# Kernel optimization log

Measured on AMD Instinct MI355X. Metric: run time of the kernel, lower is better.

Reference implementation:

```python
import jax, jax.numpy as jnp
import numpy as np

N_NODES = 100000
IN_FEATS, N_HIDDEN, N_CLASSES = 128, 128, 64
N_EDGES = 1600000


def _glorot(key, shape):
    fan_in, fan_out = shape
    lim = np.sqrt(6.0 / (fan_in + fan_out)).astype(np.float32)
    return jax.random.uniform(key, shape, jnp.float32, -lim, lim)


def setup_inputs() -> dict:
    key = jax.random.key(0)
    ks = jax.random.split(key, 12)
    x = jax.random.normal(ks[0], (N_NODES, IN_FEATS), dtype=jnp.float32)
    src = jax.random.randint(ks[1], (N_EDGES,), 0, N_NODES, dtype=jnp.int32)
    dst = jax.random.randint(ks[2], (N_EDGES,), 0, N_NODES, dtype=jnp.int32)
    dims = [(IN_FEATS, N_HIDDEN), (N_HIDDEN, N_HIDDEN), (N_HIDDEN, N_CLASSES)]
    inp = {"x": x, "src": src, "dst": dst}
    for l, (di, do) in enumerate(dims):
        inp[f"W_self{l}"] = _glorot(ks[3 + 3 * l], (di, do))
        inp[f"W_neigh{l}"] = _glorot(ks[4 + 3 * l], (di, do))
        inp[f"b{l}"] = jnp.zeros((do,), jnp.float32)
    return inp


def _sage_conv(h, src, dst, W_self, W_neigh, b):
    # mean aggregation over incoming neighbors: scatter-sum then divide by degree
    msg = h[src]                                                # [E, d]
    agg = jax.ops.segment_sum(msg, dst, num_segments=N_NODES)   # [N, d]
    deg = jax.ops.segment_sum(jnp.ones((src.shape[0],), h.dtype), dst,
                              num_segments=N_NODES)             # [N]
    h_neigh = agg / jnp.maximum(deg, 1.0)[:, None]
    return h @ W_self + h_neigh @ W_neigh + b


def reference(x, src, dst, W_self0, W_neigh0, b0, W_self1, W_neigh1, b1,
              W_self2, W_neigh2, b2):
    params = [(W_self0, W_neigh0, b0), (W_self1, W_neigh1, b1),
              (W_self2, W_neigh2, b2)]
    h = x
    n_layers = len(params)
    for i, (Ws, Wn, b) in enumerate(params):
        h = _sage_conv(h, src, dst, Ws, Wn, b)
        if i != n_layers - 1:
            h = jax.nn.relu(h)  # dropout is identity in eval mode
    return h
```

## Files before the change

kernel.cpp:

```cpp
#include <hip/hip_runtime.h>
#include <hip/hip_bf16.h>

#define N_NODES 100000
#define N_EDGES 1600000
#define PAD 64
#define FILL_SLICES 8
#define SLICE_NN (N_NODES / FILL_SLICES)
#define FILL_CHUNKS 256
#define CHUNK_E (N_EDGES / FILL_CHUNKS)

#define CVTX_BLOCKS 12500
#define CVTW_BLOCKS 320
#define CINIT_BLOCKS 391

typedef unsigned short ushort_t;
typedef unsigned int uint_t;
typedef __bf16 bf16x8 __attribute__((ext_vector_type(8)));
typedef float f32x4 __attribute__((ext_vector_type(4)));

__device__ __forceinline__ float bf2f_lo(uint_t u) {
    union { uint_t i; float f; } v; v.i = u << 16; return v.f;
}
__device__ __forceinline__ float bf2f_hi(uint_t u) {
    union { uint_t i; float f; } v; v.i = u & 0xffff0000u; return v.f;
}
__device__ __forceinline__ ushort_t f2bf(float f) {
    uint_t x = __float_as_uint(f);
    uint_t r = (x + 0x7fffu + ((x >> 16) & 1u)) >> 16;
    return (ushort_t)r;
}

#define UNPACK4(v) \
    acc[0] += bf2f_lo(v.x); acc[1] += bf2f_hi(v.x); \
    acc[2] += bf2f_lo(v.y); acc[3] += bf2f_hi(v.y); \
    acc[4] += bf2f_lo(v.z); acc[5] += bf2f_hi(v.z); \
    acc[6] += bf2f_lo(v.w); acc[7] += bf2f_hi(v.w);


__global__ __launch_bounds__(256) void k_pre(const float* __restrict__ x, ushort_t* __restrict__ h,
                                             const float* __restrict__ ws0, const float* __restrict__ wn0,
                                             const float* __restrict__ ws1, const float* __restrict__ wn1,
                                             const float* __restrict__ ws2, const float* __restrict__ wn2,
                                             ushort_t* __restrict__ wt0, ushort_t* __restrict__ wt1,
                                             ushort_t* __restrict__ wt2, int* __restrict__ cursor) {
    int b = blockIdx.x;
    if (b < CVTX_BLOCKS) {
        int i = (b * 256 + threadIdx.x) * 4;
        float4 v = *(const float4*)(x + i);
        uint2 o;
        o.x = (uint_t)f2bf(v.x) | ((uint_t)f2bf(v.y) << 16);
        o.y = (uint_t)f2bf(v.z) | ((uint_t)f2bf(v.w) << 16);
        *(uint2*)(h + i) = o;
    } else if (b < CVTX_BLOCKS + CVTW_BLOCKS) {
        int idx = (b - CVTX_BLOCKS) * 256 + threadIdx.x;
        if (idx < 65536) {
            const float* Ws = (idx < 32768) ? ws0 : ws1;
            const float* Wn = (idx < 32768) ? wn0 : wn1;
            ushort_t* Wt    = (idx < 32768) ? wt0 : wt1;
            int local = idx & 32767;
            int n = local >> 8, k = local & 255;
            float v = (k < 128) ? Ws[k * 128 + n] : Wn[(k - 128) * 128 + n];
            Wt[n * 256 + k] = f2bf(v);
        } else {
            int local = idx - 65536;
            int n = local >> 7, k = local & 127;
            float v = (n < 64) ? ws2[k * 64 + n] : wn2[k * 64 + (n - 64)];
            wt2[n * 128 + k] = f2bf(v);
        }
    } else {
        int idx = (b - CVTX_BLOCKS - CVTW_BLOCKS) * 256 + threadIdx.x;
        if (idx < N_NODES) cursor[idx] = idx * PAD;
    }
}


__global__ __launch_bounds__(256) void k_fill(const int* __restrict__ src, const int* __restrict__ dst,
                                              int* __restrict__ cursor, int* __restrict__ colp) {
    int slice = blockIdx.x & (FILL_SLICES - 1);
    int chunk = blockIdx.x >> 3;
    int lo = slice * SLICE_NN, hi = lo + SLICE_NN;
    int base = chunk * CHUNK_E;
    for (int e = base + threadIdx.x; e < base + CHUNK_E; e += 256) {
        int d = dst[e];
        if (d >= lo && d < hi) {
            int s = src[e];
            int p = atomicAdd(&cursor[d], 1);
            colp[p] = s;
        }
    }
}


__global__ __launch_bounds__(256) void k_agg(const ushort_t* __restrict__ h,
                                             const int* __restrict__ cur,
                                             const int* __restrict__ colp,
                                             ushort_t* __restrict__ out) {
    const int node = blockIdx.x * 4 + (threadIdx.x >> 6);
    const int lane = threadIdx.x & 63;
    const int j = lane >> 4;
    const int d = lane & 15;
    const int beg = node * PAD;
    const int end = cur[node];
    float acc[8];
#pragma unroll
    for (int k = 0; k < 8; ++k) acc[k] = 0.f;

    int i = beg;
    for (; i + 16 <= end; i += 16) {
        int c0 = colp[i + j];
        int c1 = colp[i + 4 + j];
        int c2 = colp[i + 8 + j];
        int c3 = colp[i + 12 + j];
        uint4 v0 = *(const uint4*)(h + (size_t)c0 * 128 + d * 8);
        uint4 v1 = *(const uint4*)(h + (size_t)c1 * 128 + d * 8);
        uint4 v2 = *(const uint4*)(h + (size_t)c2 * 128 + d * 8);
        uint4 v3 = *(const uint4*)(h + (size_t)c3 * 128 + d * 8);
        UNPACK4(v0) UNPACK4(v1) UNPACK4(v2) UNPACK4(v3)
    }
    if (i + 8 <= end) {
        int c0 = colp[i + j];
        int c1 = colp[i + 4 + j];
        uint4 v0 = *(const uint4*)(h + (size_t)c0 * 128 + d * 8);
        uint4 v1 = *(const uint4*)(h + (size_t)c1 * 128 + d * 8);
        UNPACK4(v0) UNPACK4(v1)
        i += 8;
    }
    if (i + 4 <= end) {
        int c0 = colp[i + j];
        uint4 v0 = *(const uint4*)(h + (size_t)c0 * 128 + d * 8);
        UNPACK4(v0)
        i += 4;
    }
    int rem = end - i;
    if (rem > 0) {
        int idx = i + (j < rem ? j : 0);
        int c0 = colp[idx];
        uint4 v0 = *(const uint4*)(h + (size_t)c0 * 128 + d * 8);
        if (j < rem) { UNPACK4(v0) }
    }
#pragma unroll
    for (int k = 0; k < 8; ++k) {
        acc[k] += __shfl_xor(acc[k], 16);
        acc[k] += __shfl_xor(acc[k], 32);
    }
    int deg = end - beg;
    float inv = (deg > 0) ? 1.0f / (float)deg : 0.f;
    if (lane < 16) {
        uint4 o;
        o.x = (uint_t)f2bf(acc[0] * inv) | ((uint_t)f2bf(acc[1] * inv) << 16);
        o.y = (uint_t)f2bf(acc[2] * inv) | ((uint_t)f2bf(acc[3] * inv) << 16);
        o.z = (uint_t)f2bf(acc[4] * inv) | ((uint_t)f2bf(acc[5] * inv) << 16);
        o.w = (uint_t)f2bf(acc[6] * inv) | ((uint_t)f2bf(acc[7] * inv) << 16);
        *(uint4*)(out + (size_t)node * 128 + d * 8) = o;
    }
}


__global__ __launch_bounds__(256) void k_agg_add64(const ushort_t* __restrict__ g,
                                                   const int* __restrict__ cur,
                                                   const int* __restrict__ colp,
                                                   float* __restrict__ out) {
    const int node = blockIdx.x * 4 + (threadIdx.x >> 6);
    const int lane = threadIdx.x & 63;
    const int j = lane >> 3;
    const int d = lane & 7;
    const int beg = node * PAD;
    const int end = cur[node];
    float acc[8];
#pragma unroll
    for (int k = 0; k < 8; ++k) acc[k] = 0.f;

    int i = beg;
    for (; i + 16 <= end; i += 16) {
        int c0 = colp[i + j];
        int c1 = colp[i + 8 + j];
        uint4 v0 = *(const uint4*)(g + (size_t)c0 * 64 + d * 8);
        uint4 v1 = *(const uint4*)(g + (size_t)c1 * 64 + d * 8);
        UNPACK4(v0) UNPACK4(v1)
    }
    if (i + 8 <= end) {
        int c0 = colp[i + j];
        uint4 v0 = *(const uint4*)(g + (size_t)c0 * 64 + d * 8);
        UNPACK4(v0)
        i += 8;
    }
    int rem = end - i;
    if (rem > 0) {
        int idx = i + (j < rem ? j : 0);
        int c0 = colp[idx];
        uint4 v0 = *(const uint4*)(g + (size_t)c0 * 64 + d * 8);
        if (j < rem) { UNPACK4(v0) }
    }
#pragma unroll
    for (int k = 0; k < 8; ++k) {
        acc[k] += __shfl_xor(acc[k], 8);
        acc[k] += __shfl_xor(acc[k], 16);
        acc[k] += __shfl_xor(acc[k], 32);
    }
    int deg = end - beg;
    float inv = (deg > 0) ? 1.0f / (float)deg : 0.f;
    if (lane < 8) {
        float* p = out + (size_t)node * 64 + d * 8;
        float4 p0 = *(float4*)p;
        float4 p1 = *(float4*)(p + 4);
        p0.x += acc[0] * inv; p0.y += acc[1] * inv;
        p0.z += acc[2] * inv; p0.w += acc[3] * inv;
        p1.x += acc[4] * inv; p1.y += acc[5] * inv;
        p1.z += acc[6] * inv; p1.w += acc[7] * inv;
        *(float4*)p = p0;
        *(float4*)(p + 4) = p1;
    }
}


__global__ __launch_bounds__(512) void k_gemm(const ushort_t* __restrict__ hs,
                                              const ushort_t* __restrict__ hn,
                                              const ushort_t* __restrict__ wt,
                                              const float* __restrict__ bias,
                                              ushort_t* __restrict__ hout) {
    constexpr int NT = 8;
    __shared__ ushort_t lds_w[128][264];
    const int t = threadIdx.x;
    for (int c = t; c < 128 * 32; c += 512) {
        int r = c >> 5, o = c & 31;
        *(uint4*)(&lds_w[r][o * 8]) = *(const uint4*)(wt + r * 256 + o * 8);
    }
    __syncthreads();

    int wid = t >> 6, lane = t & 63;
    int row0 = blockIdx.x * 128 + wid * 16;
    int arow = row0 + (lane & 15);
    if (arow >= N_NODES) arow = N_NODES - 1;
    int hi = lane >> 4;

    f32x4 acc[NT];
#pragma unroll
    for (int n = 0; n < NT; n++) acc[n] = (f32x4){0.f, 0.f, 0.f, 0.f};

#pragma unroll
    for (int kk = 0; kk < 8; kk++) {
        const ushort_t* hp = (kk < 4) ? hs : hn;
        int kloc = (kk & 3) * 32 + hi * 8;
        bf16x8 a = *(const bf16x8*)(hp + (size_t)arow * 128 + kloc);
#pragma unroll
        for (int n = 0; n < NT; n++) {
            bf16x8 b = *(const bf16x8*)(&lds_w[n * 16 + (lane & 15)][kk * 32 + hi * 8]);
            acc[n] = __builtin_amdgcn_mfma_f32_16x16x32_bf16(a, b, acc[n], 0, 0, 0);
        }
    }

#pragma unroll
    for (int n = 0; n < NT; n++) {
        int colc = n * 16 + (lane & 15);
        float bv = bias[colc];
#pragma unroll
        for (int j = 0; j < 4; j++) {
            int row = row0 + hi * 4 + j;
            if (row < N_NODES) {
                float v = acc[n][j] + bv;
                v = v > 0.f ? v : 0.f;
                hout[(size_t)row * 128 + colc] = f2bf(v);
            }
        }
    }
}


__global__ __launch_bounds__(512) void k_gemm2(const ushort_t* __restrict__ hs,
                                               const ushort_t* __restrict__ wt,
                                               const float* __restrict__ bias,
                                               float* __restrict__ fout,
                                               ushort_t* __restrict__ g2) {
    constexpr int NT = 8;
    __shared__ ushort_t lds_w[128][136];
    const int t = threadIdx.x;
    for (int c = t; c < 128 * 16; c += 512) {
        int r = c >> 4, o = c & 15;
        *(uint4*)(&lds_w[r][o * 8]) = *(const uint4*)(wt + r * 128 + o * 8);
    }
    __syncthreads();

    int wid = t >> 6, lane = t & 63;
    int row0 = blockIdx.x * 128 + wid * 16;
    int arow = row0 + (lane & 15);
    if (arow >= N_NODES) arow = N_NODES - 1;
    int hi = lane >> 4;

    f32x4 acc[NT];
#pragma unroll
    for (int n = 0; n < NT; n++) acc[n] = (f32x4){0.f, 0.f, 0.f, 0.f};

#pragma unroll
    for (int kk = 0; kk < 4; kk++) {
        bf16x8 a = *(const bf16x8*)(hs + (size_t)arow * 128 + kk * 32 + hi * 8);
#pragma unroll
        for (int n = 0; n < NT; n++) {
            bf16x8 b = *(const bf16x8*)(&lds_w[n * 16 + (lane & 15)][kk * 32 + hi * 8]);
            acc[n] = __builtin_amdgcn_mfma_f32_16x16x32_bf16(a, b, acc[n], 0, 0, 0);
        }
    }

#pragma unroll
    for (int n = 0; n < NT; n++) {
        int colc = n * 16 + (lane & 15);
#pragma unroll
        for (int j = 0; j < 4; j++) {
            int row = row0 + hi * 4 + j;
            if (row < N_NODES) {
                float v = acc[n][j];
                if (n < 4) fout[(size_t)row * 64 + colc] = v + bias[colc];
                else       g2[(size_t)row * 64 + (colc - 64)] = f2bf(v);
            }
        }
    }
}


extern "C" void kernel_launch(void* const* d_in, const int* in_sizes, int n_in,
                              void* d_out, int out_size, void* d_ws, size_t ws_size,
                              hipStream_t stream) {
    const float* x   = (const float*)d_in[0];
    const int*   src = (const int*)d_in[1];
    const int*   dst = (const int*)d_in[2];
    const float* ws0 = (const float*)d_in[3];
    const float* wn0 = (const float*)d_in[4];
    const float* b0  = (const float*)d_in[5];
    const float* ws1 = (const float*)d_in[6];
    const float* wn1 = (const float*)d_in[7];
    const float* b1  = (const float*)d_in[8];
    const float* ws2 = (const float*)d_in[9];
    const float* wn2 = (const float*)d_in[10];
    const float* b2  = (const float*)d_in[11];

    char* ws = (char*)d_ws;
    size_t o = 0;
    auto alloc = [&](size_t bytes) { size_t r = o; o = (o + bytes + 255) & ~(size_t)255; return r; };
    int* cursor     = (int*)(ws + alloc((size_t)N_NODES * 4));
    int* colp       = (int*)(ws + alloc((size_t)N_NODES * PAD * 4));
    ushort_t* wt0   = (ushort_t*)(ws + alloc(128 * 256 * 2));
    ushort_t* wt1   = (ushort_t*)(ws + alloc(128 * 256 * 2));
    ushort_t* wt2   = (ushort_t*)(ws + alloc(128 * 128 * 2));
    ushort_t* hA    = (ushort_t*)(ws + alloc((size_t)N_NODES * 128 * 2));
    ushort_t* hB    = (ushort_t*)(ws + alloc((size_t)N_NODES * 128 * 2));
    ushort_t* hN    = (ushort_t*)(ws + alloc((size_t)N_NODES * 128 * 2));
    (void)ws_size;

    k_pre<<<CVTX_BLOCKS + CVTW_BLOCKS + CINIT_BLOCKS, 256, 0, stream>>>(
        x, hA, ws0, wn0, ws1, wn1, ws2, wn2, wt0, wt1, wt2, cursor);
    k_fill<<<FILL_CHUNKS * FILL_SLICES, 256, 0, stream>>>(src, dst, cursor, colp);

    const int AGG_GRID  = N_NODES / 4;
    const int GEMM_GRID = (N_NODES + 127) / 128;

    k_agg<<<AGG_GRID, 256, 0, stream>>>(hA, cursor, colp, hN);
    k_gemm<<<GEMM_GRID, 512, 0, stream>>>(hA, hN, wt0, b0, hB);
    k_agg<<<AGG_GRID, 256, 0, stream>>>(hB, cursor, colp, hN);
    k_gemm<<<GEMM_GRID, 512, 0, stream>>>(hB, hN, wt1, b1, hA);
    k_gemm2<<<GEMM_GRID, 512, 0, stream>>>(hA, wt2, b2, (float*)d_out, hN);
    k_agg_add64<<<AGG_GRID, 256, 0, stream>>>(hN, cursor, colp, (float*)d_out);
}
```

Baseline: 410.4 us.

## Fuse edge fill into preprocessing kernel with memset-initialized degree counters

Replaces the sliced multi-pass fill kernel with a single pass of one thread per edge, merged into the conversion kernel. The cursor array now holds per-node degree counts, zeroed by a memset, instead of absolute offsets. Aggregation kernels compute the end index from the degree. This removes the 8x redundant reads of dst and one kernel launch, but the atomics lose the locality that slicing gave them and fill blocks share the launch with the conversion work. Neighbor order within a node is still nondeterministic.

New measurement: 480.9 us. +17.2%, slower.

```diff
diff --git a/kernel.cpp b/kernel.cpp
--- a/kernel.cpp
+++ b/kernel.cpp
@@ -4,14 +4,10 @@
 #define N_NODES 100000
 #define N_EDGES 1600000
 #define PAD 64
-#define FILL_SLICES 8
-#define SLICE_NN (N_NODES / FILL_SLICES)
-#define FILL_CHUNKS 256
-#define CHUNK_E (N_EDGES / FILL_CHUNKS)
-
+
+#define FILL_BLOCKS 6250
 #define CVTX_BLOCKS 12500
 #define CVTW_BLOCKS 320
-#define CINIT_BLOCKS 391
 
 typedef unsigned short ushort_t;
 typedef unsigned int uint_t;
@@ -37,22 +33,30 @@
     acc[6] += bf2f_lo(v.w); acc[7] += bf2f_hi(v.w);
 
 
-__global__ __launch_bounds__(256) void k_pre(const float* __restrict__ x, ushort_t* __restrict__ h,
+__global__ __launch_bounds__(256) void k_pre(const int* __restrict__ src, const int* __restrict__ dst,
+                                             int* __restrict__ cursor, int* __restrict__ colp,
+                                             const float* __restrict__ x, ushort_t* __restrict__ h,
                                              const float* __restrict__ ws0, const float* __restrict__ wn0,
                                              const float* __restrict__ ws1, const float* __restrict__ wn1,
                                              const float* __restrict__ ws2, const float* __restrict__ wn2,
                                              ushort_t* __restrict__ wt0, ushort_t* __restrict__ wt1,
-                                             ushort_t* __restrict__ wt2, int* __restrict__ cursor) {
+                                             ushort_t* __restrict__ wt2) {
     int b = blockIdx.x;
-    if (b < CVTX_BLOCKS) {
-        int i = (b * 256 + threadIdx.x) * 4;
+    if (b < FILL_BLOCKS) {
+        int e = b * 256 + threadIdx.x;
+        int d = dst[e];
+        int s = src[e];
+        int r = atomicAdd(&cursor[d], 1);
+        colp[d * PAD + r] = s;
+    } else if (b < FILL_BLOCKS + CVTX_BLOCKS) {
+        int i = ((b - FILL_BLOCKS) * 256 + threadIdx.x) * 4;
         float4 v = *(const float4*)(x + i);
         uint2 o;
         o.x = (uint_t)f2bf(v.x) | ((uint_t)f2bf(v.y) << 16);
         o.y = (uint_t)f2bf(v.z) | ((uint_t)f2bf(v.w) << 16);
         *(uint2*)(h + i) = o;
-    } else if (b < CVTX_BLOCKS + CVTW_BLOCKS) {
-        int idx = (b - CVTX_BLOCKS) * 256 + threadIdx.x;
+    } else {
+        int idx = (b - FILL_BLOCKS - CVTX_BLOCKS) * 256 + threadIdx.x;
         if (idx < 65536) {
             const float* Ws = (idx < 32768) ? ws0 : ws1;
             const float* Wn = (idx < 32768) ? wn0 : wn1;
@@ -67,26 +71,6 @@
             float v = (n < 64) ? ws2[k * 64 + n] : wn2[k * 64 + (n - 64)];
             wt2[n * 128 + k] = f2bf(v);
         }
-    } else {
-        int idx = (b - CVTX_BLOCKS - CVTW_BLOCKS) * 256 + threadIdx.x;
-        if (idx < N_NODES) cursor[idx] = idx * PAD;
-    }
-}
-
-
-__global__ __launch_bounds__(256) void k_fill(const int* __restrict__ src, const int* __restrict__ dst,
-                                              int* __restrict__ cursor, int* __restrict__ colp) {
-    int slice = blockIdx.x & (FILL_SLICES - 1);
-    int chunk = blockIdx.x >> 3;
-    int lo = slice * SLICE_NN, hi = lo + SLICE_NN;
-    int base = chunk * CHUNK_E;
-    for (int e = base + threadIdx.x; e < base + CHUNK_E; e += 256) {
-        int d = dst[e];
-        if (d >= lo && d < hi) {
-            int s = src[e];
-            int p = atomicAdd(&cursor[d], 1);
-            colp[p] = s;
-        }
     }
 }
 
@@ -100,7 +84,8 @@
     const int j = lane >> 4;
     const int d = lane & 15;
     const int beg = node * PAD;
-    const int end = cur[node];
+    const int deg = cur[node];
+    const int end = beg + deg;
     float acc[8];
 #pragma unroll
     for (int k = 0; k < 8; ++k) acc[k] = 0.f;
@@ -143,7 +128,6 @@
         acc[k] += __shfl_xor(acc[k], 16);
         acc[k] += __shfl_xor(acc[k], 32);
     }
-    int deg = end - beg;
     float inv = (deg > 0) ? 1.0f / (float)deg : 0.f;
     if (lane < 16) {
         uint4 o;
@@ -165,7 +149,8 @@
     const int j = lane >> 3;
     const int d = lane & 7;
     const int beg = node * PAD;
-    const int end = cur[node];
+    const int deg = cur[node];
+    const int end = beg + deg;
     float acc[8];
 #pragma unroll
     for (int k = 0; k < 8; ++k) acc[k] = 0.f;
@@ -197,7 +182,6 @@
         acc[k] += __shfl_xor(acc[k], 16);
         acc[k] += __shfl_xor(acc[k], 32);
     }
-    int deg = end - beg;
     float inv = (deg > 0) ? 1.0f / (float)deg : 0.f;
     if (lane < 8) {
         float* p = out + (size_t)node * 64 + d * 8;
@@ -345,9 +329,9 @@
     ushort_t* hN    = (ushort_t*)(ws + alloc((size_t)N_NODES * 128 * 2));
     (void)ws_size;
 
-    k_pre<<<CVTX_BLOCKS + CVTW_BLOCKS + CINIT_BLOCKS, 256, 0, stream>>>(
-        x, hA, ws0, wn0, ws1, wn1, ws2, wn2, wt0, wt1, wt2, cursor);
-    k_fill<<<FILL_CHUNKS * FILL_SLICES, 256, 0, stream>>>(src, dst, cursor, colp);
+    (void)hipMemsetAsync(cursor, 0, (size_t)N_NODES * 4, stream);
+    k_pre<<<FILL_BLOCKS + CVTX_BLOCKS + CVTW_BLOCKS, 256, 0, stream>>>(
+        src, dst, cursor, colp, x, hA, ws0, wn0, ws1, wn1, ws2, wn2, wt0, wt1, wt2);
 
     const int AGG_GRID  = N_NODES / 4;
     const int GEMM_GRID = (N_NODES + 127) / 128;
```
